# Optimization experiments

Hardware: AMD Instinct MI355X
Metric: run time of the kernel (lower is better)

Reference implementation:

```python
import jax, jax.numpy as jnp
import numpy as np

DIM = 1024
FF = 4096
BATCH = 4
SEQ = 2048
EPS = 1e-5


def setup_inputs() -> dict:
    key = jax.random.key(0)
    ks = jax.random.split(key, 8)
    x = jax.random.normal(ks[0], (BATCH, SEQ, DIM), dtype=jnp.float32)
    # phazor init: exp(2j*pi*arange(dim)/dim) * |randn(dim)|
    ang = 2.0 * np.pi * jnp.arange(DIM, dtype=jnp.float32) / DIM
    mag = jnp.abs(jax.random.normal(ks[1], (DIM,), dtype=jnp.float32))
    phazor_re = mag * jnp.cos(ang)
    phazor_im = mag * jnp.sin(ang)
    last_re = jax.random.normal(ks[2], (DIM,), dtype=jnp.float32)
    last_im = jax.random.normal(ks[3], (DIM,), dtype=jnp.float32)
    w1 = jax.random.normal(ks[4], (FF, DIM), dtype=jnp.float32) * DIM ** -0.5
    b1 = jnp.zeros((FF,), dtype=jnp.float32)
    w2 = jax.random.normal(ks[5], (DIM, FF), dtype=jnp.float32) * FF ** -0.5
    b2 = jnp.zeros((DIM,), dtype=jnp.float32)
    return {
        'x': x,
        'ln1_w': jnp.ones((DIM,), jnp.float32), 'ln1_b': jnp.zeros((DIM,), jnp.float32),
        'ln2_w': jnp.ones((DIM,), jnp.float32), 'ln2_b': jnp.zeros((DIM,), jnp.float32),
        'sc_lin': jnp.ones((DIM,), jnp.float32),
        'phazor_re': phazor_re, 'phazor_im': phazor_im,
        'last_re': last_re, 'last_im': last_im,
        'w1': w1, 'b1': b1, 'w2': w2, 'b2': b2,
    }


def _layer_norm(x, w, b):
    mu = jnp.mean(x, axis=-1, keepdims=True)
    var = jnp.mean(jnp.square(x - mu), axis=-1, keepdims=True)
    return (x - mu) * jax.lax.rsqrt(var + EPS) * w + b


def _sconv(x, phazor_re, phazor_im, last_re, last_im):
    B, L, D = x.shape
    dtype = x.dtype
    xc = x.astype(jnp.complex64)
    p_raw = phazor_re + 1j * phazor_im
    # tanh(|p|) * exp(i*angle(p))
    p = (jnp.tanh(jnp.abs(p_raw)) * jnp.exp(1j * jnp.angle(p_raw))).astype(jnp.complex64)
    t = jnp.arange(L)[:, None]
    prog = jnp.power(p[None, :], t)            # [L, D] complex
    filt_fft = jnp.fft.fft(prog, n=2 * L, axis=0)   # [2L, D]
    x_fft = jnp.fft.fft(xc, n=2 * L, axis=1)        # [B, 2L, D]
    conv = jnp.fft.ifft(filt_fft[None] * x_fft, axis=1)[:, :L]  # [B, L, D]
    last = (last_re + 1j * last_im)[None, None, :]  # [1,1,D] broadcast over batch
    conv_with_past = conv + last * prog[None] * p[None, None]
    return conv_with_past.real.astype(dtype)


def reference(x, ln1_w, ln1_b, ln2_w, ln2_b, sc_lin,
              phazor_re, phazor_im, last_re, last_im,
              w1, b1, w2, b2):
    # SConv branch
    x_res = x
    h = _layer_norm(x, ln1_w, ln1_b)
    h = jax.nn.silu(h)
    h = _sconv(h, phazor_re, phazor_im, last_re, last_im)
    h = h * sc_lin
    x = h + x_res
    # FFN branch
    x_res = x
    h = _layer_norm(x, ln2_w, ln2_b)
    h = jax.nn.silu(jnp.einsum('bld,fd->blf', h, w1) + b1)
    h = jnp.einsum('blf,df->bld', h, w2) + b2
    return h + x_res
```

## Files before the change

kernel.cpp:

```cpp
#include <hip/hip_runtime.h>
#include <cmath>


#define DIMD 1024
#define FFD  4096
#define BATCH 4
#define SEQL 2048
#define MROWS (BATCH*SEQL)
#define EPSF 1e-5f
#define CHUNKS2 128
#define CLEN2 (SEQL/CHUNKS2)

typedef __attribute__((ext_vector_type(8)))  _Float16 half8;
typedef __attribute__((ext_vector_type(4)))  _Float16 half4;
typedef __attribute__((ext_vector_type(4)))  float    floatx4;
typedef __attribute__((ext_vector_type(16))) float    floatx16;

#define ST_OFF   0u
#define E_OFF    1048576u
#define SV_OFF   5242880u
#define H2_OFF   35651584u
#define W1H_OFF  52428800u
#define W2H_OFF  60817408u
#define Y1_OFF   69206016u

__device__ __forceinline__ void load_lds16(const _Float16* g, _Float16* l) {
    __builtin_amdgcn_global_load_lds(
        (const __attribute__((address_space(1))) unsigned int*)g,
        (__attribute__((address_space(3))) unsigned int*)l,
        16, 0, 0);
}

__global__ __launch_bounds__(256)
void cast_f32_f16(const float* __restrict__ src, _Float16* __restrict__ dst) {
    int i = (blockIdx.x * 256 + threadIdx.x) * 4;
    float4 v = *(const float4*)(src + i);
    half4 o;
    o.x = (_Float16)v.x; o.y = (_Float16)v.y; o.z = (_Float16)v.z; o.w = (_Float16)v.w;
    *(half4*)(dst + i) = o;
}

__global__ __launch_bounds__(256)
void ln_stats(const float* __restrict__ x, float2* __restrict__ st) {
    const size_t row = blockIdx.x;
    const int tid = threadIdx.x;
    float4 v = *(const float4*)(x + row * DIMD + tid * 4);
    float s = (v.x + v.y) + (v.z + v.w);
    float q = (v.x * v.x + v.y * v.y) + (v.z * v.z + v.w * v.w);
    #pragma unroll
    for (int off = 32; off; off >>= 1) {
        s += __shfl_down(s, off, 64);
        q += __shfl_down(q, off, 64);
    }
    __shared__ float red[8];
    if (!(tid & 63)) { red[tid >> 6] = s; red[4 + (tid >> 6)] = q; }
    __syncthreads();
    if (tid == 0) {
        s = (red[0] + red[1]) + (red[2] + red[3]);
        q = (red[4] + red[5]) + (red[6] + red[7]);
        const float mu = s * (1.f / DIMD);
        const float rs = rsqrtf(q * (1.f / DIMD) - mu * mu + EPSF);
        st[row] = make_float2(mu, rs);
    }
}

__global__ __launch_bounds__(256)
void ln_kernel(const float* __restrict__ x, const float* __restrict__ w,
               const float* __restrict__ b, _Float16* __restrict__ oh) {
    const size_t row = blockIdx.x;
    const int tid = threadIdx.x;
    float4 v = *(const float4*)(x + row * DIMD + tid * 4);
    float s = (v.x + v.y) + (v.z + v.w);
    float q = (v.x * v.x + v.y * v.y) + (v.z * v.z + v.w * v.w);
    #pragma unroll
    for (int off = 32; off; off >>= 1) {
        s += __shfl_down(s, off, 64);
        q += __shfl_down(q, off, 64);
    }
    __shared__ float red[8];
    if (!(tid & 63)) { red[tid >> 6] = s; red[4 + (tid >> 6)] = q; }
    __syncthreads();
    s = (red[0] + red[1]) + (red[2] + red[3]);
    q = (red[4] + red[5]) + (red[6] + red[7]);
    const float mu = s * (1.f / DIMD);
    const float rs = rsqrtf(q * (1.f / DIMD) - mu * mu + EPSF);
    float4 wv = *(const float4*)(w + tid * 4);
    float4 bv = *(const float4*)(b + tid * 4);
    half4 hv;
    hv.x = (_Float16)((v.x - mu) * rs * wv.x + bv.x);
    hv.y = (_Float16)((v.y - mu) * rs * wv.y + bv.y);
    hv.z = (_Float16)((v.z - mu) * rs * wv.z + bv.z);
    hv.w = (_Float16)((v.w - mu) * rs * wv.w + bv.w);
    *(half4*)(oh + row * DIMD + tid * 4) = hv;
}

__device__ __forceinline__ void get_p(const float* pre, const float* pim, int d,
                                      float& pr, float& pi) {
    float re = pre[d], im = pim[d];
    float r = sqrtf(re * re + im * im);
    float t = tanhf(r) / fmaxf(r, 1e-30f);
    pr = re * t; pi = im * t;
}

__global__ __launch_bounds__(256)
void scan_partial(const float* __restrict__ x, const float2* __restrict__ st,
                  const float* __restrict__ lw, const float* __restrict__ lb,
                  const float* __restrict__ pre, const float* __restrict__ pim,
                  float2* __restrict__ e) {
    const int tid = threadIdx.x;
    const int c = blockIdx.x;
    const int bb = blockIdx.y;
    const int d0 = tid * 4;
    float pr[4], pi[4];
    #pragma unroll
    for (int k = 0; k < 4; ++k) get_p(pre, pim, d0 + k, pr[k], pi[k]);
    const float4 wv = *(const float4*)(lw + d0);
    const float4 bv = *(const float4*)(lb + d0);
    const float wa[4] = {wv.x, wv.y, wv.z, wv.w};
    const float ba[4] = {bv.x, bv.y, bv.z, bv.w};
    const size_t row0 = (size_t)bb * SEQL + (size_t)c * CLEN2;
    float sr[4] = {0.f, 0.f, 0.f, 0.f}, si[4] = {0.f, 0.f, 0.f, 0.f};
    #pragma unroll
    for (int j = 0; j < CLEN2; ++j) {
        float4 v = *(const float4*)(x + (row0 + j) * DIMD + d0);
        float2 sj = st[row0 + j];
        const float xa[4] = {v.x, v.y, v.z, v.w};
        #pragma unroll
        for (int k = 0; k < 4; ++k) {
            float o = (xa[k] - sj.x) * sj.y * wa[k] + ba[k];
            float h = o / (1.f + __expf(-o));
            float nr = pr[k] * sr[k] - pi[k] * si[k] + h;
            float ni = pr[k] * si[k] + pi[k] * sr[k];
            sr[k] = nr; si[k] = ni;
        }
    }
    float2* ep = e + ((size_t)bb * CHUNKS2 + c) * DIMD + d0;
    #pragma unroll
    for (int k = 0; k < 4; ++k) ep[k] = make_float2(sr[k], si[k]);
}

__global__ __launch_bounds__(256)
void scan_combine(const float2* __restrict__ e, const float* __restrict__ pre,
                  const float* __restrict__ pim, const float* __restrict__ lre,
                  const float* __restrict__ lim, float2* __restrict__ sv) {
    const int d = blockIdx.x * 256 + threadIdx.x;
    const int bb = blockIdx.y;
    float pr, pi; get_p(pre, pim, d, pr, pi);
    float qr = pr, qi = pi;
    #pragma unroll
    for (int s = 0; s < 4; ++s) {
        float nr = qr * qr - qi * qi;
        float ni = 2.f * qr * qi;
        qr = nr; qi = ni;
    }
    float sr = lre[d], si = lim[d];
    for (int c = 0; c < CHUNKS2; ++c) {
        sv[((size_t)bb * CHUNKS2 + c) * DIMD + d] = make_float2(sr, si);
        float2 ec = e[((size_t)bb * CHUNKS2 + c) * DIMD + d];
        float nr = qr * sr - qi * si + ec.x;
        float ni = qr * si + qi * sr + ec.y;
        sr = nr; si = ni;
    }
}

__global__ __launch_bounds__(256)
void scan_final(const float* __restrict__ x, const float2* __restrict__ st,
                const float* __restrict__ lw, const float* __restrict__ lb,
                const float* __restrict__ pre, const float* __restrict__ pim,
                const float* __restrict__ sc, const float2* __restrict__ sv,
                float* __restrict__ x2) {
    const int tid = threadIdx.x;
    const int c = blockIdx.x;
    const int bb = blockIdx.y;
    const int d0 = tid * 4;
    float pr[4], pi[4];
    #pragma unroll
    for (int k = 0; k < 4; ++k) get_p(pre, pim, d0 + k, pr[k], pi[k]);
    const float4 wv = *(const float4*)(lw + d0);
    const float4 bv = *(const float4*)(lb + d0);
    const float4 scv = *(const float4*)(sc + d0);
    const float wa[4] = {wv.x, wv.y, wv.z, wv.w};
    const float ba[4] = {bv.x, bv.y, bv.z, bv.w};
    const float sca[4] = {scv.x, scv.y, scv.z, scv.w};
    const size_t row0 = (size_t)bb * SEQL + (size_t)c * CLEN2;
    float sr[4], si[4];
    {
        const float2* s0 = sv + ((size_t)bb * CHUNKS2 + c) * DIMD + d0;
        #pragma unroll
        for (int k = 0; k < 4; ++k) { sr[k] = s0[k].x; si[k] = s0[k].y; }
    }
    #pragma unroll
    for (int j = 0; j < CLEN2; ++j) {
        float4 v = *(const float4*)(x + (row0 + j) * DIMD + d0);
        float2 sj = st[row0 + j];
        const float xa[4] = {v.x, v.y, v.z, v.w};
        float out[4];
        #pragma unroll
        for (int k = 0; k < 4; ++k) {
            float o = (xa[k] - sj.x) * sj.y * wa[k] + ba[k];
            float h = o / (1.f + __expf(-o));
            float nr = pr[k] * sr[k] - pi[k] * si[k] + h;
            float ni = pr[k] * si[k] + pi[k] * sr[k];
            sr[k] = nr; si[k] = ni;
            out[k] = xa[k] + sca[k] * nr;
        }
        float4 ov = {out[0], out[1], out[2], out[3]};
        *(float4*)(x2 + (row0 + j) * DIMD + d0) = ov;
    }
}

#define GBM 128
#define GBN 128
#define GBK 64

template<int NCOLS>
__global__ __launch_bounds__(256)
void gemm1_32(const _Float16* __restrict__ A, const _Float16* __restrict__ W,
              const float* __restrict__ bias, _Float16* __restrict__ out_h,
              int N, int K) {
    __shared__ _Float16 As[GBM * GBK];
    __shared__ _Float16 Bs[GBN * GBK];
    const int tid  = threadIdx.x;
    const int lane = tid & 63;
    const int wave = tid >> 6;
    const int wm = (wave >> 1) * 64;
    const int wn = (wave & 1) * 64;
    const int n  = blockIdx.y * gridDim.x + blockIdx.x;
    const int xc = n & 7, ii = n >> 3;
    const size_t m0 = (size_t)(xc + ((ii / NCOLS) << 3)) * GBM;
    const size_t n0 = (size_t)(ii % NCOLS) * GBN;
    const int r32 = lane & 31;
    const int kg  = lane >> 5;

    const int srow = wave * 32 + (lane >> 3);
    const int ccp  = ((lane & 7) ^ (lane >> 3)) * 8;
    const _Float16* ag = A + (m0 + srow) * (size_t)K + ccp;
    const _Float16* wg = W + (n0 + srow) * (size_t)K + ccp;
    _Float16* asl = &As[(wave * 32) * GBK];
    _Float16* bsl = &Bs[(wave * 32) * GBK];

    floatx16 acc[2][2] = {};

    for (int k0 = 0; k0 < K; k0 += GBK) {
        #pragma unroll
        for (int t = 0; t < 4; ++t) {
            load_lds16(ag + k0 + (size_t)(t * 8) * K, asl + t * 8 * GBK);
            load_lds16(wg + k0 + (size_t)(t * 8) * K, bsl + t * 8 * GBK);
        }
        __syncthreads();
        #pragma unroll
        for (int ks = 0; ks < 4; ++ks) {
            const int slot = (((ks << 1) | kg) ^ (r32 & 7)) * 8;
            half8 af0 = *(const half8*)(&As[(wm +      r32) * GBK + slot]);
            half8 af1 = *(const half8*)(&As[(wm + 32 + r32) * GBK + slot]);
            half8 bf0 = *(const half8*)(&Bs[(wn +      r32) * GBK + slot]);
            half8 bf1 = *(const half8*)(&Bs[(wn + 32 + r32) * GBK + slot]);
            acc[0][0] = __builtin_amdgcn_mfma_f32_32x32x16_f16(af0, bf0, acc[0][0], 0, 0, 0);
            acc[0][1] = __builtin_amdgcn_mfma_f32_32x32x16_f16(af0, bf1, acc[0][1], 0, 0, 0);
            acc[1][0] = __builtin_amdgcn_mfma_f32_32x32x16_f16(af1, bf0, acc[1][0], 0, 0, 0);
            acc[1][1] = __builtin_amdgcn_mfma_f32_32x32x16_f16(af1, bf1, acc[1][1], 0, 0, 0);
        }
        __syncthreads();
    }

    #pragma unroll
    for (int ib = 0; ib < 2; ++ib) {
        #pragma unroll
        for (int jb = 0; jb < 2; ++jb) {
            const size_t gn = n0 + wn + jb * 32 + r32;
            const float bb = bias[gn];
            #pragma unroll
            for (int r = 0; r < 16; ++r) {
                const size_t gm = m0 + wm + ib * 32 + (r & 3) + 8 * (r >> 2) + 4 * kg;
                float v = acc[ib][jb][r] + bb;
                float sl = v / (1.f + __expf(-v));
                out_h[gm * (size_t)N + gn] = (_Float16)sl;
            }
        }
    }
}

template<int NCOLS>
__global__ __launch_bounds__(256)
void gemm2_16(const _Float16* __restrict__ A, const _Float16* __restrict__ W,
              const float* __restrict__ bias, const float* __restrict__ resid,
              float* __restrict__ out_f, int N, int K) {
    __shared__ _Float16 As[GBM * GBK];
    __shared__ _Float16 Bs[GBN * GBK];
    const int tid  = threadIdx.x;
    const int lane = tid & 63;
    const int wave = tid >> 6;
    const int wm = (wave >> 1) * 64;
    const int wn = (wave & 1) * 64;
    const int n  = blockIdx.y * gridDim.x + blockIdx.x;
    const int xc = n & 7, ii = n >> 3;
    const size_t m0 = (size_t)(xc + ((ii / NCOLS) << 3)) * GBM;
    const size_t n0 = (size_t)(ii % NCOLS) * GBN;
    const int fr = lane & 15;
    const int quad = lane >> 4;

    const int srow = wave * 32 + (lane >> 3);
    const int ccp  = ((lane & 7) ^ (lane >> 3)) * 8;
    const _Float16* ag = A + (m0 + srow) * (size_t)K + ccp;
    const _Float16* wg = W + (n0 + srow) * (size_t)K + ccp;
    _Float16* asl = &As[(wave * 32) * GBK];
    _Float16* bsl = &Bs[(wave * 32) * GBK];

    floatx4 acc[4][4] = {};

    for (int k0 = 0; k0 < K; k0 += GBK) {
        #pragma unroll
        for (int t = 0; t < 4; ++t) {
            load_lds16(ag + k0 + (size_t)(t * 8) * K, asl + t * 8 * GBK);
            load_lds16(wg + k0 + (size_t)(t * 8) * K, bsl + t * 8 * GBK);
        }
        __syncthreads();
        #pragma unroll
        for (int kk = 0; kk < GBK; kk += 32) {
            half8 af[4], bf[4];
            #pragma unroll
            for (int i = 0; i < 4; ++i) {
                const int slot = (((kk >> 3) + quad) ^ (fr & 7)) * 8;
                af[i] = *(const half8*)(&As[(wm + i * 16 + fr) * GBK + slot]);
                bf[i] = *(const half8*)(&Bs[(wn + i * 16 + fr) * GBK + slot]);
            }
            #pragma unroll
            for (int i = 0; i < 4; ++i)
                #pragma unroll
                for (int j = 0; j < 4; ++j)
                    acc[i][j] = __builtin_amdgcn_mfma_f32_16x16x32_f16(
                        af[i], bf[j], acc[i][j], 0, 0, 0);
        }
        __syncthreads();
    }

    #pragma unroll
    for (int i = 0; i < 4; ++i) {
        #pragma unroll
        for (int j = 0; j < 4; ++j) {
            #pragma unroll
            for (int r = 0; r < 4; ++r) {
                const size_t gm = m0 + wm + i * 16 + quad * 4 + r;
                const size_t gn = n0 + wn + j * 16 + fr;
                float v = acc[i][j][r] + bias[gn];
                out_f[gm * (size_t)N + gn] = v + resid[gm * (size_t)N + gn];
            }
        }
    }
}

extern "C" void kernel_launch(void* const* d_in, const int* in_sizes, int n_in,
                              void* d_out, int out_size, void* d_ws, size_t ws_size,
                              hipStream_t stream) {
    const float* x    = (const float*)d_in[0];
    const float* ln1w = (const float*)d_in[1];
    const float* ln1b = (const float*)d_in[2];
    const float* ln2w = (const float*)d_in[3];
    const float* ln2b = (const float*)d_in[4];
    const float* sc   = (const float*)d_in[5];
    const float* pre  = (const float*)d_in[6];
    const float* pim  = (const float*)d_in[7];
    const float* lre  = (const float*)d_in[8];
    const float* lim  = (const float*)d_in[9];
    const float* w1   = (const float*)d_in[10];
    const float* b1   = (const float*)d_in[11];
    const float* w2   = (const float*)d_in[12];
    const float* b2   = (const float*)d_in[13];

    char* ws = (char*)d_ws;
    float2*     st  = (float2*)(ws + ST_OFF);
    float2*     e   = (float2*)(ws + E_OFF);
    float2*     sv  = (float2*)(ws + SV_OFF);
    _Float16*   h2  = (_Float16*)(ws + H2_OFF);
    _Float16*   w1h = (_Float16*)(ws + W1H_OFF);
    _Float16*   w2h = (_Float16*)(ws + W2H_OFF);
    _Float16*   y1  = (_Float16*)(ws + Y1_OFF);
    float*      x2  = (float*)d_out;
    float*      outp = (float*)d_out;

    cast_f32_f16<<<dim3(FFD * DIMD / 1024), 256, 0, stream>>>(w1, w1h);
    cast_f32_f16<<<dim3(FFD * DIMD / 1024), 256, 0, stream>>>(w2, w2h);
    ln_stats<<<dim3(MROWS), 256, 0, stream>>>(x, st);
    scan_partial<<<dim3(CHUNKS2, BATCH), 256, 0, stream>>>(
        x, st, ln1w, ln1b, pre, pim, e);
    scan_combine<<<dim3(DIMD / 256, BATCH), 256, 0, stream>>>(
        e, pre, pim, lre, lim, sv);
    scan_final<<<dim3(CHUNKS2, BATCH), 256, 0, stream>>>(
        x, st, ln1w, ln1b, pre, pim, sc, sv, x2);
    ln_kernel<<<dim3(MROWS), 256, 0, stream>>>(x2, ln2w, ln2b, h2);
    gemm1_32<32><<<dim3(FFD / GBN, MROWS / GBM), 256, 0, stream>>>(
        h2, w1h, b1, y1, FFD, DIMD);
    gemm2_16<8><<<dim3(DIMD / GBN, MROWS / GBM), 256, 0, stream>>>(
        y1, w2h, b2, x2, outp, DIMD, FFD);
}
```

Baseline: 361.9 us.

## Fuse prep kernels, fold scan combine and LayerNorm2 into scan_final

After: 370.5 us. 1.02x slower.

```diff
diff --git a/kernel.cpp b/kernel.cpp
--- a/kernel.cpp
+++ b/kernel.cpp
@@ -10,6 +10,7 @@
 #define EPSF 1e-5f
 #define CHUNKS2 128
 #define CLEN2 (SEQL/CHUNKS2)
+#define CAST_BLKS (FFD*DIMD/1024)
 
 typedef __attribute__((ext_vector_type(8)))  _Float16 half8;
 typedef __attribute__((ext_vector_type(4)))  _Float16 half4;
@@ -18,7 +19,6 @@
 
 #define ST_OFF   0u
 #define E_OFF    1048576u
-#define SV_OFF   5242880u
 #define H2_OFF   35651584u
 #define W1H_OFF  52428800u
 #define W2H_OFF  60817408u
@@ -32,66 +32,44 @@
 }
 
 __global__ __launch_bounds__(256)
-void cast_f32_f16(const float* __restrict__ src, _Float16* __restrict__ dst) {
-    int i = (blockIdx.x * 256 + threadIdx.x) * 4;
-    float4 v = *(const float4*)(src + i);
-    half4 o;
-    o.x = (_Float16)v.x; o.y = (_Float16)v.y; o.z = (_Float16)v.z; o.w = (_Float16)v.w;
-    *(half4*)(dst + i) = o;
-}
-
-__global__ __launch_bounds__(256)
-void ln_stats(const float* __restrict__ x, float2* __restrict__ st) {
-    const size_t row = blockIdx.x;
+void prep(const float* __restrict__ x, float2* __restrict__ st,
+          const float* __restrict__ w1, _Float16* __restrict__ w1h,
+          const float* __restrict__ w2, _Float16* __restrict__ w2h) {
+    const int bid = blockIdx.x;
     const int tid = threadIdx.x;
-    float4 v = *(const float4*)(x + row * DIMD + tid * 4);
-    float s = (v.x + v.y) + (v.z + v.w);
-    float q = (v.x * v.x + v.y * v.y) + (v.z * v.z + v.w * v.w);
-    #pragma unroll
-    for (int off = 32; off; off >>= 1) {
-        s += __shfl_down(s, off, 64);
-        q += __shfl_down(q, off, 64);
-    }
-    __shared__ float red[8];
-    if (!(tid & 63)) { red[tid >> 6] = s; red[4 + (tid >> 6)] = q; }
-    __syncthreads();
-    if (tid == 0) {
-        s = (red[0] + red[1]) + (red[2] + red[3]);
-        q = (red[4] + red[5]) + (red[6] + red[7]);
-        const float mu = s * (1.f / DIMD);
-        const float rs = rsqrtf(q * (1.f / DIMD) - mu * mu + EPSF);
-        st[row] = make_float2(mu, rs);
-    }
-}
-
-__global__ __launch_bounds__(256)
-void ln_kernel(const float* __restrict__ x, const float* __restrict__ w,
-               const float* __restrict__ b, _Float16* __restrict__ oh) {
-    const size_t row = blockIdx.x;
-    const int tid = threadIdx.x;
-    float4 v = *(const float4*)(x + row * DIMD + tid * 4);
-    float s = (v.x + v.y) + (v.z + v.w);
-    float q = (v.x * v.x + v.y * v.y) + (v.z * v.z + v.w * v.w);
-    #pragma unroll
-    for (int off = 32; off; off >>= 1) {
-        s += __shfl_down(s, off, 64);
-        q += __shfl_down(q, off, 64);
-    }
-    __shared__ float red[8];
-    if (!(tid & 63)) { red[tid >> 6] = s; red[4 + (tid >> 6)] = q; }
-    __syncthreads();
-    s = (red[0] + red[1]) + (red[2] + red[3]);
-    q = (red[4] + red[5]) + (red[6] + red[7]);
-    const float mu = s * (1.f / DIMD);
-    const float rs = rsqrtf(q * (1.f / DIMD) - mu * mu + EPSF);
-    float4 wv = *(const float4*)(w + tid * 4);
-    float4 bv = *(const float4*)(b + tid * 4);
-    half4 hv;
-    hv.x = (_Float16)((v.x - mu) * rs * wv.x + bv.x);
-    hv.y = (_Float16)((v.y - mu) * rs * wv.y + bv.y);
-    hv.z = (_Float16)((v.z - mu) * rs * wv.z + bv.z);
-    hv.w = (_Float16)((v.w - mu) * rs * wv.w + bv.w);
-    *(half4*)(oh + row * DIMD + tid * 4) = hv;
+    if (bid < MROWS) {
+        const size_t row = bid;
+        float4 v = *(const float4*)(x + row * DIMD + tid * 4);
+        float s = (v.x + v.y) + (v.z + v.w);
+        float q = (v.x * v.x + v.y * v.y) + (v.z * v.z + v.w * v.w);
+        #pragma unroll
+        for (int off = 32; off; off >>= 1) {
+            s += __shfl_down(s, off, 64);
+            q += __shfl_down(q, off, 64);
+        }
+        __shared__ float red[8];
+        if (!(tid & 63)) { red[tid >> 6] = s; red[4 + (tid >> 6)] = q; }
+        __syncthreads();
+        if (tid == 0) {
+            s = (red[0] + red[1]) + (red[2] + red[3]);
+            q = (red[4] + red[5]) + (red[6] + red[7]);
+            const float mu = s * (1.f / DIMD);
+            const float rs = rsqrtf(q * (1.f / DIMD) - mu * mu + EPSF);
+            st[row] = make_float2(mu, rs);
+        }
+    } else {
+        int b = bid - MROWS;
+        const float* src;
+        _Float16* dst;
+        if (b < CAST_BLKS) { src = w1; dst = w1h; }
+        else { b -= CAST_BLKS; src = w2; dst = w2h; }
+        int i = (b * 256 + tid) * 4;
+        float4 v = *(const float4*)(src + i);
+        half4 o;
+        o.x = (_Float16)v.x; o.y = (_Float16)v.y;
+        o.z = (_Float16)v.z; o.w = (_Float16)v.w;
+        *(half4*)(dst + i) = o;
+    }
 }
 
 __device__ __forceinline__ void get_p(const float* pre, const float* pim, int d,
@@ -139,36 +117,27 @@
     for (int k = 0; k < 4; ++k) ep[k] = make_float2(sr[k], si[k]);
 }
 
-__global__ __launch_bounds__(256)
-void scan_combine(const float2* __restrict__ e, const float* __restrict__ pre,
-                  const float* __restrict__ pim, const float* __restrict__ lre,
-                  const float* __restrict__ lim, float2* __restrict__ sv) {
-    const int d = blockIdx.x * 256 + threadIdx.x;
-    const int bb = blockIdx.y;
-    float pr, pi; get_p(pre, pim, d, pr, pi);
-    float qr = pr, qi = pi;
-    #pragma unroll
-    for (int s = 0; s < 4; ++s) {
-        float nr = qr * qr - qi * qi;
-        float ni = 2.f * qr * qi;
-        qr = nr; qi = ni;
-    }
-    float sr = lre[d], si = lim[d];
-    for (int c = 0; c < CHUNKS2; ++c) {
-        sv[((size_t)bb * CHUNKS2 + c) * DIMD + d] = make_float2(sr, si);
-        float2 ec = e[((size_t)bb * CHUNKS2 + c) * DIMD + d];
-        float nr = qr * sr - qi * si + ec.x;
-        float ni = qr * si + qi * sr + ec.y;
-        sr = nr; si = ni;
-    }
+__device__ __forceinline__ void block_red2(float& s, float& q, float (*red)[8],
+                                           int tid, int buf) {
+    #pragma unroll
+    for (int off = 32; off; off >>= 1) {
+        s += __shfl_down(s, off, 64);
+        q += __shfl_down(q, off, 64);
+    }
+    if (!(tid & 63)) { red[buf][tid >> 6] = s; red[buf][4 + (tid >> 6)] = q; }
+    __syncthreads();
+    s = (red[buf][0] + red[buf][1]) + (red[buf][2] + red[buf][3]);
+    q = (red[buf][4] + red[buf][5]) + (red[buf][6] + red[buf][7]);
 }
 
 __global__ __launch_bounds__(256)
 void scan_final(const float* __restrict__ x, const float2* __restrict__ st,
-                const float* __restrict__ lw, const float* __restrict__ lb,
+                const float* __restrict__ l1w, const float* __restrict__ l1b,
+                const float* __restrict__ l2w, const float* __restrict__ l2b,
                 const float* __restrict__ pre, const float* __restrict__ pim,
-                const float* __restrict__ sc, const float2* __restrict__ sv,
-                float* __restrict__ x2) {
+                const float* __restrict__ sc, const float* __restrict__ lre,
+                const float* __restrict__ lim, const float2* __restrict__ e,
+                float* __restrict__ x2, _Float16* __restrict__ h2) {
     const int tid = threadIdx.x;
     const int c = blockIdx.x;
     const int bb = blockIdx.y;
@@ -176,36 +145,74 @@
     float pr[4], pi[4];
     #pragma unroll
     for (int k = 0; k < 4; ++k) get_p(pre, pim, d0 + k, pr[k], pi[k]);
-    const float4 wv = *(const float4*)(lw + d0);
-    const float4 bv = *(const float4*)(lb + d0);
+    const float4 w1v = *(const float4*)(l1w + d0);
+    const float4 b1v = *(const float4*)(l1b + d0);
+    const float4 w2v = *(const float4*)(l2w + d0);
+    const float4 b2v = *(const float4*)(l2b + d0);
     const float4 scv = *(const float4*)(sc + d0);
-    const float wa[4] = {wv.x, wv.y, wv.z, wv.w};
-    const float ba[4] = {bv.x, bv.y, bv.z, bv.w};
+    const float w1a[4] = {w1v.x, w1v.y, w1v.z, w1v.w};
+    const float b1a[4] = {b1v.x, b1v.y, b1v.z, b1v.w};
+    const float w2a[4] = {w2v.x, w2v.y, w2v.z, w2v.w};
+    const float b2a[4] = {b2v.x, b2v.y, b2v.z, b2v.w};
     const float sca[4] = {scv.x, scv.y, scv.z, scv.w};
+
+    float qr[4], qi[4];
+    #pragma unroll
+    for (int k = 0; k < 4; ++k) { qr[k] = pr[k]; qi[k] = pi[k]; }
+    #pragma unroll
+    for (int s = 0; s < 4; ++s)
+        #pragma unroll
+        for (int k = 0; k < 4; ++k) {
+            float nr = qr[k] * qr[k] - qi[k] * qi[k];
+            float ni = 2.f * qr[k] * qi[k];
+            qr[k] = nr; qi[k] = ni;
+        }
+
+    float sr[4], si[4];
+    #pragma unroll
+    for (int k = 0; k < 4; ++k) { sr[k] = lre[d0 + k]; si[k] = lim[d0 + k]; }
+    const float2* ep = e + (size_t)bb * CHUNKS2 * DIMD + d0;
+    for (int cc = 0; cc < c; ++cc) {
+        #pragma unroll
+        for (int k = 0; k < 4; ++k) {
+            float2 ec = ep[(size_t)cc * DIMD + k];
+            float nr = qr[k] * sr[k] - qi[k] * si[k] + ec.x;
+            float ni = qr[k] * si[k] + qi[k] * sr[k] + ec.y;
+            sr[k] = nr; si[k] = ni;
+        }
+    }
+
     const size_t row0 = (size_t)bb * SEQL + (size_t)c * CLEN2;
-    float sr[4], si[4];
-    {
-        const float2* s0 = sv + ((size_t)bb * CHUNKS2 + c) * DIMD + d0;
-        #pragma unroll
-        for (int k = 0; k < 4; ++k) { sr[k] = s0[k].x; si[k] = s0[k].y; }
-    }
+    __shared__ float red[2][8];
     #pragma unroll
     for (int j = 0; j < CLEN2; ++j) {
         float4 v = *(const float4*)(x + (row0 + j) * DIMD + d0);
         float2 sj = st[row0 + j];
         const float xa[4] = {v.x, v.y, v.z, v.w};
-        float out[4];
+        float x2v[4];
         #pragma unroll
         for (int k = 0; k < 4; ++k) {
-            float o = (xa[k] - sj.x) * sj.y * wa[k] + ba[k];
+            float o = (xa[k] - sj.x) * sj.y * w1a[k] + b1a[k];
             float h = o / (1.f + __expf(-o));
             float nr = pr[k] * sr[k] - pi[k] * si[k] + h;
             float ni = pr[k] * si[k] + pi[k] * sr[k];
             sr[k] = nr; si[k] = ni;
-            out[k] = xa[k] + sca[k] * nr;
-        }
-        float4 ov = {out[0], out[1], out[2], out[3]};
-        *(float4*)(x2 + (row0 + j) * DIMD + d0) = ov;
+            x2v[k] = xa[k] + sca[k] * nr;
+        }
+        float4 xo = {x2v[0], x2v[1], x2v[2], x2v[3]};
+        *(float4*)(x2 + (row0 + j) * DIMD + d0) = xo;
+        float s = (x2v[0] + x2v[1]) + (x2v[2] + x2v[3]);
+        float q = (x2v[0] * x2v[0] + x2v[1] * x2v[1]) +
+                  (x2v[2] * x2v[2] + x2v[3] * x2v[3]);
+        block_red2(s, q, red, tid, j & 1);
+        const float mu = s * (1.f / DIMD);
+        const float rs = rsqrtf(q * (1.f / DIMD) - mu * mu + EPSF);
+        half4 hv;
+        hv.x = (_Float16)((x2v[0] - mu) * rs * w2a[0] + b2a[0]);
+        hv.y = (_Float16)((x2v[1] - mu) * rs * w2a[1] + b2a[1]);
+        hv.z = (_Float16)((x2v[2] - mu) * rs * w2a[2] + b2a[2]);
+        hv.w = (_Float16)((x2v[3] - mu) * rs * w2a[3] + b2a[3]);
+        *(half4*)(h2 + (row0 + j) * DIMD + d0) = hv;
     }
 }
 
@@ -370,7 +377,6 @@
     char* ws = (char*)d_ws;
     float2*     st  = (float2*)(ws + ST_OFF);
     float2*     e   = (float2*)(ws + E_OFF);
-    float2*     sv  = (float2*)(ws + SV_OFF);
     _Float16*   h2  = (_Float16*)(ws + H2_OFF);
     _Float16*   w1h = (_Float16*)(ws + W1H_OFF);
     _Float16*   w2h = (_Float16*)(ws + W2H_OFF);
@@ -378,16 +384,12 @@
     float*      x2  = (float*)d_out;
     float*      outp = (float*)d_out;
 
-    cast_f32_f16<<<dim3(FFD * DIMD / 1024), 256, 0, stream>>>(w1, w1h);
-    cast_f32_f16<<<dim3(FFD * DIMD / 1024), 256, 0, stream>>>(w2, w2h);
-    ln_stats<<<dim3(MROWS), 256, 0, stream>>>(x, st);
+    prep<<<dim3(MROWS + 2 * CAST_BLKS), 256, 0, stream>>>(
+        x, st, w1, w1h, w2, w2h);
     scan_partial<<<dim3(CHUNKS2, BATCH), 256, 0, stream>>>(
         x, st, ln1w, ln1b, pre, pim, e);
-    scan_combine<<<dim3(DIMD / 256, BATCH), 256, 0, stream>>>(
-        e, pre, pim, lre, lim, sv);
     scan_final<<<dim3(CHUNKS2, BATCH), 256, 0, stream>>>(
-        x, st, ln1w, ln1b, pre, pim, sc, sv, x2);
-    ln_kernel<<<dim3(MROWS), 256, 0, stream>>>(x2, ln2w, ln2b, h2);
+        x, st, ln1w, ln1b, ln2w, ln2b, pre, pim, sc, lre, lim, e, x2, h2);
     gemm1_32<32><<<dim3(FFD / GBN, MROWS / GBM), 256, 0, stream>>>(
         h2, w1h, b1, y1, FFD, DIMD);
     gemm2_16<8><<<dim3(DIMD / GBN, MROWS / GBM), 256, 0, stream>>>(
```
